# Kernel tuning notes

Measured on AMD Instinct MI355X. Metric: run time of the kernel, lower is better.

The kernel has to match this reference:

```python
import jax, jax.numpy as jnp
import numpy as np
from jax.scipy.special import logsumexp

TEMPERATURE = 0.7
N_ITERS = 8


def setup_inputs() -> dict:
    key = jax.random.key(0)
    k1, k2, k3 = jax.random.split(key, 3)
    b, n, d = 4, 8192, 1024
    num_tokens = 1024
    x = jax.random.normal(k1, (b, n, d), dtype=jnp.float32)
    routing_token = jax.random.normal(k2, (d,), dtype=jnp.float32)
    # gumbel noise: -log(-log(u)), u ~ U(0,1)
    u = jax.random.uniform(k3, (b, num_tokens, n), dtype=jnp.float32, minval=1e-20, maxval=1.0)
    gumbel = -jnp.log(jnp.clip(-jnp.log(u), 1e-20))
    mask = jnp.ones((b, n), dtype=bool)
    return {"x": x, "routing_token": routing_token, "gumbel": gumbel, "mask": mask, "num_tokens": num_tokens}


def _sinkhorn(t, n_iters=N_ITERS):
    # alternating row/col log-normalization, then exp
    def body(t, _):
        t = t - logsumexp(t, axis=-2, keepdims=True)
        t = t - logsumexp(t, axis=-1, keepdims=True)
        return t, None
    t, _ = jax.lax.scan(body, t, None, length=n_iters)
    return jnp.exp(t)


def reference(x, routing_token, gumbel, mask, num_tokens):
    b, n, d = x.shape
    mask_value = -jnp.finfo(x.dtype).max
    scores = jnp.einsum('bnd,d->bn', x, routing_token)              # [b, n]
    scores = jnp.broadcast_to(scores[:, None, :], (b, num_tokens, n))  # [b, num_tokens, n]
    smask = mask[:, None, :]                                        # [b, 1, n]
    scores = jnp.where(smask, scores, mask_value)
    # gumbel sinkhorn
    t = scores / TEMPERATURE + gumbel
    t = _sinkhorn(t)
    t = jnp.where(smask, t, mask_value)
    # topk(1) along token axis j
    selected_scores = jnp.max(t, axis=-1)                           # [b, num_tokens]
    selected_indices = jnp.argmax(t, axis=-1)                       # [b, num_tokens]
    # straight-through: forward value 1.0, gradient via selected_scores
    selected_scores = selected_scores + jax.lax.stop_gradient(1.0 - selected_scores)
    selected_mask = jnp.take_along_axis(mask, selected_indices, axis=1)
    selected_scores = jnp.where(selected_mask, selected_scores, 0.0)
    return selected_scores, selected_indices
```

## Files before the change

### kernel.cpp

```cpp
#include <hip/hip_runtime.h>
#include <math.h>

#define B 4
#define N 8192
#define K 1024
#define ROWS 16
#define KB (K / ROWS)
#define TPB 512

__device__ __forceinline__ void lse_step(float v, float& m, float& s) {
  float nm = fmaxf(m, v);
  s = s * __expf(m - nm) + __expf(v - nm);
  m = nm;
}
__device__ __forceinline__ void lse_merge(float m2, float s2, float& m, float& s) {
  float nm = fmaxf(m, m2);
  s = s * __expf(m - nm) + s2 * __expf(m2 - nm);
  m = nm;
}

__global__ __launch_bounds__(TPB) void col0_kernel(const float* __restrict__ g,
                                                   float* __restrict__ part) {
  int kb = blockIdx.x, b = blockIdx.y;
  const float* gbase = g + ((size_t)(b * K + kb * ROWS)) * N;
  int t = threadIdx.x;
  float cm[4][4], cs[4][4];
#pragma unroll
  for (int j = 0; j < 4; ++j)
#pragma unroll
    for (int q = 0; q < 4; ++q) { cm[j][q] = -INFINITY; cs[j][q] = 0.f; }
  for (int rI = 0; rI < ROWS; ++rI) {
    const float* gr = gbase + (size_t)rI * N;
#pragma unroll
    for (int j = 0; j < 4; ++j) {
      float4 gv = *(const float4*)(gr + j * 2048 + t * 4);
      lse_step(gv.x, cm[j][0], cs[j][0]);
      lse_step(gv.y, cm[j][1], cs[j][1]);
      lse_step(gv.z, cm[j][2], cs[j][2]);
      lse_step(gv.w, cm[j][3], cs[j][3]);
    }
  }
  float* pp = part + ((size_t)(kb * B + b)) * N;
#pragma unroll
  for (int j = 0; j < 4; ++j) {
    float4 o = make_float4(cm[j][0] + __logf(cs[j][0]), cm[j][1] + __logf(cs[j][1]),
                           cm[j][2] + __logf(cs[j][2]), cm[j][3] + __logf(cs[j][3]));
    *(float4*)(pp + j * 2048 + t * 4) = o;
  }
}

__global__ __launch_bounds__(256) void combine_kernel(const float* __restrict__ part,
                                                      float* __restrict__ d) {
  int idx = blockIdx.x * 256 + threadIdx.x;
  float m = -INFINITY, s = 0.f;
  for (int p = 0; p < KB; ++p) lse_step(part[(size_t)p * (B * N) + idx], m, s);
  d[idx] = -(m + __logf(s));
}

__global__ __launch_bounds__(TPB) void fused_kernel(const float* __restrict__ g,
                                                    const float* __restrict__ d,
                                                    float* __restrict__ part) {
  int kb = blockIdx.x, b = blockIdx.y;
  const float* gbase = g + ((size_t)(b * K + kb * ROWS)) * N;
  const float* dp = d + b * N;
  int t = threadIdx.x;
  int lane = t & 63, wv = t >> 6;

  __shared__ float2 wpart[ROWS][TPB / 64];
  __shared__ float rnew[ROWS];

  for (int rI = 0; rI < ROWS; ++rI) {
    const float* gr = gbase + (size_t)rI * N;
    float m = -INFINITY, s = 0.f;
#pragma unroll
    for (int j = 0; j < 4; ++j) {
      int n = j * 2048 + t * 4;
      float4 gv = *(const float4*)(gr + n);
      float4 dv = *(const float4*)(dp + n);
      lse_step(gv.x + dv.x, m, s);
      lse_step(gv.y + dv.y, m, s);
      lse_step(gv.z + dv.z, m, s);
      lse_step(gv.w + dv.w, m, s);
    }
#pragma unroll
    for (int off = 32; off; off >>= 1) {
      float m2 = __shfl_down(m, off, 64);
      float s2 = __shfl_down(s, off, 64);
      lse_merge(m2, s2, m, s);
    }
    if (lane == 0) wpart[rI][wv] = make_float2(m, s);
  }
  __syncthreads();
  if (t < ROWS) {
    float m = -INFINITY, s = 0.f;
#pragma unroll
    for (int w = 0; w < TPB / 64; ++w) lse_merge(wpart[t][w].x, wpart[t][w].y, m, s);
    rnew[t] = m + __logf(s);
  }
  __syncthreads();

  float cm[4][4], cs[4][4];
#pragma unroll
  for (int j = 0; j < 4; ++j)
#pragma unroll
    for (int q = 0; q < 4; ++q) { cm[j][q] = -INFINITY; cs[j][q] = 0.f; }
  for (int rI = 0; rI < ROWS; ++rI) {
    float rk = rnew[rI];
    const float* gr = gbase + (size_t)rI * N;
#pragma unroll
    for (int j = 0; j < 4; ++j) {
      float4 gv = *(const float4*)(gr + j * 2048 + t * 4);
      lse_step(gv.x - rk, cm[j][0], cs[j][0]);
      lse_step(gv.y - rk, cm[j][1], cs[j][1]);
      lse_step(gv.z - rk, cm[j][2], cs[j][2]);
      lse_step(gv.w - rk, cm[j][3], cs[j][3]);
    }
  }
  float* pp = part + ((size_t)(kb * B + b)) * N;
#pragma unroll
  for (int j = 0; j < 4; ++j) {
    float4 o = make_float4(cm[j][0] + __logf(cs[j][0]), cm[j][1] + __logf(cs[j][1]),
                           cm[j][2] + __logf(cs[j][2]), cm[j][3] + __logf(cs[j][3]));
    *(float4*)(pp + j * 2048 + t * 4) = o;
  }
}

__global__ __launch_bounds__(256) void argmax_kernel(const float* __restrict__ g,
                                                     const float* __restrict__ d,
                                                     float* __restrict__ out) {
  int row = blockIdx.x;
  int b = row >> 10;
  const float* gp = g + (size_t)row * N;
  const float* dp = d + b * N;
  float bv = -INFINITY;
  int bi = 0;
#pragma unroll
  for (int j = 0; j < 8; ++j) {
    int n = j * 1024 + threadIdx.x * 4;
    float4 gv = *(const float4*)(gp + n);
    float4 dv = *(const float4*)(dp + n);
    float v;
    v = gv.x + dv.x; if (v > bv) { bv = v; bi = n + 0; }
    v = gv.y + dv.y; if (v > bv) { bv = v; bi = n + 1; }
    v = gv.z + dv.z; if (v > bv) { bv = v; bi = n + 2; }
    v = gv.w + dv.w; if (v > bv) { bv = v; bi = n + 3; }
  }
  __shared__ float svv[256];
  __shared__ int sii[256];
  svv[threadIdx.x] = bv;
  sii[threadIdx.x] = bi;
  __syncthreads();
  for (int off = 128; off > 0; off >>= 1) {
    if (threadIdx.x < off) {
      float v2 = svv[threadIdx.x + off];
      int i2 = sii[threadIdx.x + off];
      float v1 = svv[threadIdx.x];
      int i1 = sii[threadIdx.x];
      if (v2 > v1 || (v2 == v1 && i2 < i1)) {
        svv[threadIdx.x] = v2;
        sii[threadIdx.x] = i2;
      }
    }
    __syncthreads();
  }
  if (threadIdx.x == 0) {
    out[row] = 1.0f;
    out[B * K + row] = (float)sii[0];
  }
}

extern "C" void kernel_launch(void* const* d_in, const int* in_sizes, int n_in,
                              void* d_out, int out_size, void* d_ws, size_t ws_size,
                              hipStream_t stream) {
  const float* g = (const float*)d_in[2];
  float* out = (float*)d_out;

  char* ws = (char*)d_ws;
  float* d = (float*)ws;
  float* part = (float*)(ws + (1 << 20));

  col0_kernel<<<dim3(KB, B), TPB, 0, stream>>>(g, part);
  combine_kernel<<<B * N / 256, 256, 0, stream>>>(part, d);
  for (int it = 0; it < 7; ++it) {
    fused_kernel<<<dim3(KB, B), TPB, 0, stream>>>(g, d, part);
    combine_kernel<<<B * N / 256, 256, 0, stream>>>(part, d);
  }
  argmax_kernel<<<B * K, 256, 0, stream>>>(g, d, out);
}
```

Measured before the change: 615.1 us.

## Fuse all Sinkhorn iterations into one cooperative kernel with grid syncs

Replaces the sequence of column, combine, fused and argmax kernels with a single persistent cooperative kernel of 256 blocks that uses grid.sync between phases. It also drops the running-max log-sum-exp in favour of plain exp sums, relying on the bounded input range, and processes row pairs with block reductions. Argmax is folded into the final phase. This removes about 17 kernel launches and their gaps but adds grid-wide barriers, reduces parallelism to one 1024-thread block per CU, and risks overflow if values grow large.

Result: slower. 971.4 us (+57.9%).

```diff
diff --git a/kernel.cpp b/kernel.cpp
--- a/kernel.cpp
+++ b/kernel.cpp
@@ -1,171 +1,169 @@
 #include <hip/hip_runtime.h>
+#include <hip/hip_cooperative_groups.h>
 #include <math.h>
+
+namespace cg = cooperative_groups;
 
 #define B 4
 #define N 8192
 #define K 1024
+#define TPB 1024
+#define GRID 256
 #define ROWS 16
-#define KB (K / ROWS)
-#define TPB 512
+#define KG 64
 
-__device__ __forceinline__ void lse_step(float v, float& m, float& s) {
-  float nm = fmaxf(m, v);
-  s = s * __expf(m - nm) + __expf(v - nm);
-  m = nm;
-}
-__device__ __forceinline__ void lse_merge(float m2, float s2, float& m, float& s) {
-  float nm = fmaxf(m, m2);
-  s = s * __expf(m - nm) + s2 * __expf(m2 - nm);
-  m = nm;
-}
 
-__global__ __launch_bounds__(TPB) void col0_kernel(const float* __restrict__ g,
-                                                   float* __restrict__ part) {
-  int kb = blockIdx.x, b = blockIdx.y;
-  const float* gbase = g + ((size_t)(b * K + kb * ROWS)) * N;
+__global__ __launch_bounds__(TPB, 1) void mega_kernel(
+    const float* __restrict__ g, float* __restrict__ part,
+    float* __restrict__ d, float* __restrict__ out) {
+  cg::grid_group grid = cg::this_grid();
+  int bi = blockIdx.x;
+  int b = bi >> 6;
+  int kg = bi & 63;
   int t = threadIdx.x;
-  float cm[4][4], cs[4][4];
-#pragma unroll
-  for (int j = 0; j < 4; ++j)
-#pragma unroll
-    for (int q = 0; q < 4; ++q) { cm[j][q] = -INFINITY; cs[j][q] = 0.f; }
+  int lane = t & 63, wv = t >> 6;
+
+  const float* gbase = g + ((size_t)(b * K + kg * ROWS)) * N;
+  float* pp = part + ((size_t)(kg * B + b)) * N;
+  const float* dp = d + b * N;
+
+  __shared__ float r_lds[ROWS];
+  __shared__ float red[2][16];
+  __shared__ float avv[16];
+  __shared__ int aii[16];
+
+  float scol[2][4] = {{0.f, 0.f, 0.f, 0.f}, {0.f, 0.f, 0.f, 0.f}};
   for (int rI = 0; rI < ROWS; ++rI) {
     const float* gr = gbase + (size_t)rI * N;
 #pragma unroll
-    for (int j = 0; j < 4; ++j) {
-      float4 gv = *(const float4*)(gr + j * 2048 + t * 4);
-      lse_step(gv.x, cm[j][0], cs[j][0]);
-      lse_step(gv.y, cm[j][1], cs[j][1]);
-      lse_step(gv.z, cm[j][2], cs[j][2]);
-      lse_step(gv.w, cm[j][3], cs[j][3]);
+    for (int j = 0; j < 2; ++j) {
+      float4 gv = *(const float4*)(gr + j * 4096 + t * 4);
+      scol[j][0] += __expf(gv.x);
+      scol[j][1] += __expf(gv.y);
+      scol[j][2] += __expf(gv.z);
+      scol[j][3] += __expf(gv.w);
     }
   }
-  float* pp = part + ((size_t)(kb * B + b)) * N;
 #pragma unroll
-  for (int j = 0; j < 4; ++j) {
-    float4 o = make_float4(cm[j][0] + __logf(cs[j][0]), cm[j][1] + __logf(cs[j][1]),
-                           cm[j][2] + __logf(cs[j][2]), cm[j][3] + __logf(cs[j][3]));
-    *(float4*)(pp + j * 2048 + t * 4) = o;
+  for (int j = 0; j < 2; ++j) {
+    float4 o = make_float4(__logf(scol[j][0]), __logf(scol[j][1]),
+                           __logf(scol[j][2]), __logf(scol[j][3]));
+    *(float4*)(pp + j * 4096 + t * 4) = o;
   }
-}
+  if (t < ROWS) r_lds[t] = 0.f;
+  grid.sync();
 
-__global__ __launch_bounds__(256) void combine_kernel(const float* __restrict__ part,
-                                                      float* __restrict__ d) {
-  int idx = blockIdx.x * 256 + threadIdx.x;
-  float m = -INFINITY, s = 0.f;
-  for (int p = 0; p < KB; ++p) lse_step(part[(size_t)p * (B * N) + idx], m, s);
-  d[idx] = -(m + __logf(s));
-}
+  for (int it = 0; it < 8; ++it) {
+    int gid = bi * TPB + t;
+    if (gid < B * N) {
+      float s = 0.f;
+      const float* q = part + gid;
+#pragma unroll 8
+      for (int p = 0; p < KG; ++p) s += __expf(q[(size_t)p * (B * N)]);
+      d[gid] = -__logf(s);
+    }
+    grid.sync();
+    if (it == 7) break;
 
-__global__ __launch_bounds__(TPB) void fused_kernel(const float* __restrict__ g,
-                                                    const float* __restrict__ d,
-                                                    float* __restrict__ part) {
-  int kb = blockIdx.x, b = blockIdx.y;
-  const float* gbase = g + ((size_t)(b * K + kb * ROWS)) * N;
-  const float* dp = d + b * N;
-  int t = threadIdx.x;
-  int lane = t & 63, wv = t >> 6;
+    float dreg[2][4];
+#pragma unroll
+    for (int j = 0; j < 2; ++j) {
+      float4 dv = *(const float4*)(dp + j * 4096 + t * 4);
+      dreg[j][0] = dv.x; dreg[j][1] = dv.y; dreg[j][2] = dv.z; dreg[j][3] = dv.w;
+    }
+    scol[0][0] = scol[0][1] = scol[0][2] = scol[0][3] = 0.f;
+    scol[1][0] = scol[1][1] = scol[1][2] = scol[1][3] = 0.f;
+    for (int sc = 0; sc < ROWS / 2; ++sc) {
+      int k0 = sc * 2, k1 = k0 + 1;
+      const float* gr0 = gbase + (size_t)k0 * N;
+      const float* gr1 = gbase + (size_t)k1 * N;
+      float ga[2][4], gb[2][4];
+#pragma unroll
+      for (int j = 0; j < 2; ++j) {
+        float4 v0 = *(const float4*)(gr0 + j * 4096 + t * 4);
+        float4 v1 = *(const float4*)(gr1 + j * 4096 + t * 4);
+        ga[j][0] = v0.x; ga[j][1] = v0.y; ga[j][2] = v0.z; ga[j][3] = v0.w;
+        gb[j][0] = v1.x; gb[j][1] = v1.y; gb[j][2] = v1.z; gb[j][3] = v1.w;
+      }
+      float M0 = r_lds[k0], M1 = r_lds[k1];
+      float sa = 0.f, sb = 0.f;
+#pragma unroll
+      for (int j = 0; j < 2; ++j)
+#pragma unroll
+        for (int q = 0; q < 4; ++q) {
+          sa += __expf(ga[j][q] + dreg[j][q] - M0);
+          sb += __expf(gb[j][q] + dreg[j][q] - M1);
+        }
+#pragma unroll
+      for (int off = 32; off; off >>= 1) {
+        sa += __shfl_down(sa, off, 64);
+        sb += __shfl_down(sb, off, 64);
+      }
+      if (lane == 0) { red[0][wv] = sa; red[1][wv] = sb; }
+      __syncthreads();
+      if (t == 0) {
+        float A = 0.f, Bs = 0.f;
+#pragma unroll
+        for (int w = 0; w < 16; ++w) { A += red[0][w]; Bs += red[1][w]; }
+        r_lds[k0] = M0 + __logf(A);
+        r_lds[k1] = M1 + __logf(Bs);
+      }
+      __syncthreads();
+      float r0 = r_lds[k0], r1 = r_lds[k1];
+#pragma unroll
+      for (int j = 0; j < 2; ++j)
+#pragma unroll
+        for (int q = 0; q < 4; ++q)
+          scol[j][q] += __expf(ga[j][q] - r0) + __expf(gb[j][q] - r1);
+    }
+#pragma unroll
+    for (int j = 0; j < 2; ++j) {
+      float4 o = make_float4(__logf(scol[j][0]), __logf(scol[j][1]),
+                             __logf(scol[j][2]), __logf(scol[j][3]));
+      *(float4*)(pp + j * 4096 + t * 4) = o;
+    }
+    grid.sync();
+  }
 
-  __shared__ float2 wpart[ROWS][TPB / 64];
-  __shared__ float rnew[ROWS];
-
+  float dreg[2][4];
+#pragma unroll
+  for (int j = 0; j < 2; ++j) {
+    float4 dv = *(const float4*)(dp + j * 4096 + t * 4);
+    dreg[j][0] = dv.x; dreg[j][1] = dv.y; dreg[j][2] = dv.z; dreg[j][3] = dv.w;
+  }
   for (int rI = 0; rI < ROWS; ++rI) {
     const float* gr = gbase + (size_t)rI * N;
-    float m = -INFINITY, s = 0.f;
+    float bv = -INFINITY;
+    int bidx = 0;
 #pragma unroll
-    for (int j = 0; j < 4; ++j) {
-      int n = j * 2048 + t * 4;
+    for (int j = 0; j < 2; ++j) {
+      int n = j * 4096 + t * 4;
       float4 gv = *(const float4*)(gr + n);
-      float4 dv = *(const float4*)(dp + n);
-      lse_step(gv.x + dv.x, m, s);
-      lse_step(gv.y + dv.y, m, s);
-      lse_step(gv.z + dv.z, m, s);
-      lse_step(gv.w + dv.w, m, s);
+      float v;
+      v = gv.x + dreg[j][0]; if (v > bv) { bv = v; bidx = n; }
+      v = gv.y + dreg[j][1]; if (v > bv) { bv = v; bidx = n + 1; }
+      v = gv.z + dreg[j][2]; if (v > bv) { bv = v; bidx = n + 2; }
+      v = gv.w + dreg[j][3]; if (v > bv) { bv = v; bidx = n + 3; }
     }
 #pragma unroll
     for (int off = 32; off; off >>= 1) {
-      float m2 = __shfl_down(m, off, 64);
-      float s2 = __shfl_down(s, off, 64);
-      lse_merge(m2, s2, m, s);
+      float v2 = __shfl_down(bv, off, 64);
+      int i2 = __shfl_down(bidx, off, 64);
+      if (v2 > bv || (v2 == bv && i2 < bidx)) { bv = v2; bidx = i2; }
     }
-    if (lane == 0) wpart[rI][wv] = make_float2(m, s);
-  }
-  __syncthreads();
-  if (t < ROWS) {
-    float m = -INFINITY, s = 0.f;
+    if (lane == 0) { avv[wv] = bv; aii[wv] = bidx; }
+    __syncthreads();
+    if (t == 0) {
+      float fv = avv[0];
+      int fi = aii[0];
 #pragma unroll
-    for (int w = 0; w < TPB / 64; ++w) lse_merge(wpart[t][w].x, wpart[t][w].y, m, s);
-    rnew[t] = m + __logf(s);
-  }
-  __syncthreads();
-
-  float cm[4][4], cs[4][4];
-#pragma unroll
-  for (int j = 0; j < 4; ++j)
-#pragma unroll
-    for (int q = 0; q < 4; ++q) { cm[j][q] = -INFINITY; cs[j][q] = 0.f; }
-  for (int rI = 0; rI < ROWS; ++rI) {
-    float rk = rnew[rI];
-    const float* gr = gbase + (size_t)rI * N;
-#pragma unroll
-    for (int j = 0; j < 4; ++j) {
-      float4 gv = *(const float4*)(gr + j * 2048 + t * 4);
-      lse_step(gv.x - rk, cm[j][0], cs[j][0]);
-      lse_step(gv.y - rk, cm[j][1], cs[j][1]);
-      lse_step(gv.z - rk, cm[j][2], cs[j][2]);
-      lse_step(gv.w - rk, cm[j][3], cs[j][3]);
-    }
-  }
-  float* pp = part + ((size_t)(kb * B + b)) * N;
-#pragma unroll
-  for (int j = 0; j < 4; ++j) {
-    float4 o = make_float4(cm[j][0] + __logf(cs[j][0]), cm[j][1] + __logf(cs[j][1]),
-                           cm[j][2] + __logf(cs[j][2]), cm[j][3] + __logf(cs[j][3]));
-    *(float4*)(pp + j * 2048 + t * 4) = o;
-  }
-}
-
-__global__ __launch_bounds__(256) void argmax_kernel(const float* __restrict__ g,
-                                                     const float* __restrict__ d,
-                                                     float* __restrict__ out) {
-  int row = blockIdx.x;
-  int b = row >> 10;
-  const float* gp = g + (size_t)row * N;
-  const float* dp = d + b * N;
-  float bv = -INFINITY;
-  int bi = 0;
-#pragma unroll
-  for (int j = 0; j < 8; ++j) {
-    int n = j * 1024 + threadIdx.x * 4;
-    float4 gv = *(const float4*)(gp + n);
-    float4 dv = *(const float4*)(dp + n);
-    float v;
-    v = gv.x + dv.x; if (v > bv) { bv = v; bi = n + 0; }
-    v = gv.y + dv.y; if (v > bv) { bv = v; bi = n + 1; }
-    v = gv.z + dv.z; if (v > bv) { bv = v; bi = n + 2; }
-    v = gv.w + dv.w; if (v > bv) { bv = v; bi = n + 3; }
-  }
-  __shared__ float svv[256];
-  __shared__ int sii[256];
-  svv[threadIdx.x] = bv;
-  sii[threadIdx.x] = bi;
-  __syncthreads();
-  for (int off = 128; off > 0; off >>= 1) {
-    if (threadIdx.x < off) {
-      float v2 = svv[threadIdx.x + off];
-      int i2 = sii[threadIdx.x + off];
-      float v1 = svv[threadIdx.x];
-      int i1 = sii[threadIdx.x];
-      if (v2 > v1 || (v2 == v1 && i2 < i1)) {
-        svv[threadIdx.x] = v2;
-        sii[threadIdx.x] = i2;
-      }
+      for (int w = 1; w < 16; ++w)
+        if (avv[w] > fv || (avv[w] == fv && aii[w] < fi)) { fv = avv[w]; fi = aii[w]; }
+      int row = b * K + kg * ROWS + rI;
+      out[row] = 1.0f;
+      out[B * K + row] = (float)fi;
     }
     __syncthreads();
-  }
-  if (threadIdx.x == 0) {
-    out[row] = 1.0f;
-    out[B * K + row] = (float)sii[0];
   }
 }
 
@@ -176,14 +174,10 @@
   float* out = (float*)d_out;
 
   char* ws = (char*)d_ws;
-  float* d = (float*)ws;
-  float* part = (float*)(ws + (1 << 20));
+  float* part = (float*)ws;
+  float* d = (float*)(ws + (16u << 20));
 
-  col0_kernel<<<dim3(KB, B), TPB, 0, stream>>>(g, part);
-  combine_kernel<<<B * N / 256, 256, 0, stream>>>(part, d);
-  for (int it = 0; it < 7; ++it) {
-    fused_kernel<<<dim3(KB, B), TPB, 0, stream>>>(g, d, part);
-    combine_kernel<<<B * N / 256, 256, 0, stream>>>(part, d);
-  }
-  argmax_kernel<<<B * K, 256, 0, stream>>>(g, d, out);
+  void* args[] = {(void*)&g, (void*)&part, (void*)&d, (void*)&out};
+  hipLaunchCooperativeKernel((void*)mega_kernel, dim3(GRID), dim3(TPB), args, 0,
+                             stream);
 }
```
